# Kernel tuning notes

Hardware: AMD Instinct MI355X
Metric: run time of the kernel (lower is better)

The kernel has to match this reference:

```python
import jax, jax.numpy as jnp
import numpy as np

CHEB = jnp.array([676.5203681218851, -1259.1392167224028, 771.3234287776531,
                  -176.6150291621406, 12.507343278686905, -0.13857109526572012,
                  9.984369578019572e-06, 1.5056327351493116e-07], dtype=jnp.float32)
TWO_PI = float(np.sqrt(2.0 * np.pi))  # sqrt(2*pi), matches torch two_pi constant


def _gamma(z):
    # Lanczos approximation, 8 Chebyshev terms
    x = jnp.full_like(z, 0.9999999999998099)
    for i in range(8):
        x = x + CHEB[i] / (z + (i + 1.0))
    t = z + 8.0 - 0.5
    y = TWO_PI * t ** (z + 0.5) * jnp.exp(-t) * x
    return y / z


def _lower_incl_gamma(s, x, iters=8):
    it = iters - 2
    gs = _gamma(s)
    L = x ** s * gs * jnp.exp(-x)
    gs = gs * s
    R = jnp.reciprocal(gs) * jnp.ones_like(x)
    X = x
    for k in range(it):
        gs = gs * (s + k + 1)
        R = R + X / gs
        X = X * x
    gs = gs * (s + it + 1)
    R = R + X / gs
    return L * R


def _trigamma(x):
    z = x + 1.0
    zz = z * z
    a = 0.2 - jnp.reciprocal(7.0 * zz)
    b = 1.0 - a / zz
    c = 1.0 + b / (3.0 * z)
    d = 1.0 + c / (2.0 * z)
    return d / z + jnp.reciprocal(x * x)


def _k_update(k, s):
    nm = jnp.log(k) - jax.scipy.special.digamma(k) - s
    dn = jnp.reciprocal(k) - _trigamma(k)
    return k - nm / dn


def _compute_ml_est(x, i=10):
    # x: [B, N]; returns per-image k, th of shape [B]
    x = x + 1e-07
    mean_x = jnp.mean(x, axis=1)
    s = jnp.log(mean_x) - jnp.mean(jnp.log(x), axis=1)
    s3 = s - 3.0
    rt = jnp.sqrt(s3 * s3 + 24.0 * s)
    k = (3.0 - s + rt) / (12.0 * s) + 1e-07
    for _ in range(i):
        k = _k_update(k, s)
    k = jnp.clip(k, 1e-07, 18.0)
    th = jnp.reciprocal(k) * mean_x
    return k, th


def setup_inputs() -> dict:
    key = jax.random.key(0)
    x = jax.random.uniform(key, (256, 224, 224), dtype=jnp.float32)
    return {"x": x}


def reference(x):
    B, H, W = x.shape
    xf = x.reshape(B, H * W)
    xf = xf - jnp.min(xf, axis=1, keepdims=True) + 1e-07
    k, th = _compute_ml_est(xf)            # [B], [B]
    kb = k[:, None]                         # broadcast per-image stats over pixels
    y = jnp.reciprocal(_gamma(kb)) * _lower_incl_gamma(kb, xf / th[:, None])
    y = jnp.where(jnp.isfinite(y), y, jnp.zeros_like(y))
    return y.reshape(B, H, W)
```

## Files before the change

### kernel.cpp

```cpp
#include <hip/hip_runtime.h>
#include <math.h>

#define HW   50176
#define NV4  12544
#define TPB  1024

__device__ __forceinline__ float waveReduceMin(float v) {
#pragma unroll
    for (int o = 32; o > 0; o >>= 1) v = fminf(v, __shfl_down(v, o, 64));
    return v;
}
__device__ __forceinline__ double waveReduceSum(double v) {
#pragma unroll
    for (int o = 32; o > 0; o >>= 1) v += __shfl_down(v, o, 64);
    return v;
}

__device__ __forceinline__ float digamma_f(float x) {
    float r = 0.0f;
    while (x < 6.0f) { r -= 1.0f / x; x += 1.0f; }
    float f = 1.0f / (x * x);
    float ser = f * (1.0f/12.0f - f * (1.0f/120.0f - f * (1.0f/252.0f - f * (1.0f/240.0f - f * (1.0f/132.0f)))));
    return r + logf(x) - 0.5f / x - ser;
}

__device__ __forceinline__ float trigamma_ref(float x) {
    float z = x + 1.0f;
    float zz = z * z;
    float a = 0.2f - 1.0f / (7.0f * zz);
    float b = 1.0f - a / zz;
    float c = 1.0f + b / (3.0f * z);
    float d = 1.0f + c / (2.0f * z);
    return d / z + 1.0f / (x * x);
}

__global__ void __launch_bounds__(TPB)
gamma_norm2d(const float* __restrict__ x, float* __restrict__ out) {
    const int row = blockIdx.x;
    const int tid = threadIdx.x;
    const float4* __restrict__ xr = (const float4*)(x + (size_t)row * HW);
    float4* __restrict__ yr = (float4*)(out + (size_t)row * HW);

    const bool lastValid = (tid < (NV4 - 12 * TPB));

    float4 v[13];
#pragma unroll
    for (int j = 0; j < 12; ++j) v[j] = xr[tid + j * TPB];
    if (lastValid) v[12] = xr[tid + 12 * TPB];
    else           v[12] = make_float4(INFINITY, INFINITY, INFINITY, INFINITY);

    float m = INFINITY;
#pragma unroll
    for (int j = 0; j < 13; ++j)
        m = fminf(m, fminf(fminf(v[j].x, v[j].y), fminf(v[j].z, v[j].w)));
    m = waveReduceMin(m);

    __shared__ float  sminw[16];
    __shared__ double ssum[16], ssuml[16];
    __shared__ float  sparams[3];
    __shared__ float  scoef[8];

    const int wid = tid >> 6, lane = tid & 63;
    if (lane == 0) sminw[wid] = m;
    __syncthreads();
    if (tid == 0) {
        float mm = sminw[0];
        for (int i = 1; i < 16; ++i) mm = fminf(mm, sminw[i]);
        sparams[0] = mm;
    }
    __syncthreads();
    const float rmin = sparams[0];

    double lsum = 0.0, lsl = 0.0;
#pragma unroll
    for (int j = 0; j < 13; ++j) {
        if (j < 12 || lastValid) {
            float e0 = v[j].x, e1 = v[j].y, e2 = v[j].z, e3 = v[j].w;
            float xm0 = (e0 - rmin + 1e-7f) + 1e-7f;
            float xm1 = (e1 - rmin + 1e-7f) + 1e-7f;
            float xm2 = (e2 - rmin + 1e-7f) + 1e-7f;
            float xm3 = (e3 - rmin + 1e-7f) + 1e-7f;
            lsum += ((double)xm0 + (double)xm1) + ((double)xm2 + (double)xm3);
            lsl  += ((double)__logf(xm0) + (double)__logf(xm1))
                  + ((double)__logf(xm2) + (double)__logf(xm3));
        }
    }
    lsum = waveReduceSum(lsum);
    lsl  = waveReduceSum(lsl);
    if (lane == 0) { ssum[wid] = lsum; ssuml[wid] = lsl; }
    __syncthreads();

    if (tid == 0) {
        double ts = 0.0, tl = 0.0;
        for (int i = 0; i < 16; ++i) { ts += ssum[i]; tl += ssuml[i]; }
        const double meand = ts / (double)HW;
        const double mlogd = tl / (double)HW;
        float s = (float)(log(meand) - mlogd);

        float s3 = s - 3.0f;
        float rt = sqrtf(s3 * s3 + 24.0f * s);
        float k  = (3.0f - s + rt) / (12.0f * s) + 1e-7f;
        for (int it = 0; it < 10; ++it) {
            float nm = logf(k) - digamma_f(k) - s;
            float dn = 1.0f / k - trigamma_ref(k);
            k = k - nm / dn;
        }
        if (k < 1e-7f) k = 1e-7f;
        if (k > 18.0f) k = 18.0f;

        const double CH[8] = {676.5203681218851, -1259.1392167224028, 771.3234287776531,
                              -176.6150291621406, 12.507343278686905, -0.13857109526572012,
                              9.984369578019572e-06, 1.5056327351493116e-07};
        double z = (double)k;
        double acc = 0.9999999999998099;
        for (int i = 0; i < 8; ++i) acc += CH[i] / (z + (double)(i + 1));
        double t = z + 7.5;
        double g = 2.5066282746310002 * exp((z + 0.5) * log(t) - t) * acc / z;

        double den = g * z;
        scoef[0] = (float)(1.0 / den);
        for (int j = 1; j < 8; ++j) {
            den *= (z + (double)j);
            scoef[j] = (float)(1.0 / den);
        }
        sparams[1] = k;
        sparams[2] = (float)((double)k / meand);
    }
    __syncthreads();

    const float kk    = sparams[1];
    const float invth = sparams[2];
    const float c0 = scoef[0], c1 = scoef[1], c2 = scoef[2], c3 = scoef[3];
    const float c4 = scoef[4], c5 = scoef[5], c6 = scoef[6], c7 = scoef[7];

#pragma unroll
    for (int j = 0; j < 13; ++j) {
        if (j < 12 || lastValid) {
            float e[4] = {v[j].x, v[j].y, v[j].z, v[j].w};
            float o[4];
#pragma unroll
            for (int q = 0; q < 4; ++q) {
                float xf = e[q] - rmin + 1e-7f;
                float xq = xf * invth;
                float p = fmaf(c7, xq, c6);
                p = fmaf(p, xq, c5);
                p = fmaf(p, xq, c4);
                p = fmaf(p, xq, c3);
                p = fmaf(p, xq, c2);
                p = fmaf(p, xq, c1);
                p = fmaf(p, xq, c0);
                float tt = __expf(fmaf(kk, __logf(xq), -xq));
                float y = tt * p;
                o[q] = isfinite(y) ? y : 0.0f;
            }
            yr[tid + j * TPB] = make_float4(o[0], o[1], o[2], o[3]);
        }
    }
}

extern "C" void kernel_launch(void* const* d_in, const int* in_sizes, int n_in,
                              void* d_out, int out_size, void* d_ws, size_t ws_size,
                              hipStream_t stream) {
    const float* x = (const float*)d_in[0];
    float* out = (float*)d_out;
    const int rows = in_sizes[0] / HW;
    gamma_norm2d<<<dim3(rows), dim3(TPB), 0, stream>>>(x, out);
}
```

Baseline: 113.6 us.

## Use float accumulation, fuse raw sum into min pass, fast divides, nontemporal stores

Replaces the per-element double-precision sum and log-sum accumulation with float accumulation per thread, converting to double only for the wave reductions. The plain sum is computed during the min pass and shifted by the row minimum afterward, which removes one dependency. The serial k-estimation and gamma code on thread 0 switches to fast divides and single-precision exp/log, and output stores become nontemporal. The aim is to cut FP64 ALU work and the single-thread serial section, at the cost of some accuracy in the mean and the gamma coefficients.

```diff
diff --git a/kernel.cpp b/kernel.cpp
--- a/kernel.cpp
+++ b/kernel.cpp
@@ -5,12 +5,14 @@
 #define NV4  12544
 #define TPB  1024
 
-__device__ __forceinline__ float waveReduceMin(float v) {
+typedef float floatx4 __attribute__((ext_vector_type(4)));
+
+__device__ __forceinline__ float waveMin(float v) {
 #pragma unroll
     for (int o = 32; o > 0; o >>= 1) v = fminf(v, __shfl_down(v, o, 64));
     return v;
 }
-__device__ __forceinline__ double waveReduceSum(double v) {
+__device__ __forceinline__ double waveSumD(double v) {
 #pragma unroll
     for (int o = 32; o > 0; o >>= 1) v += __shfl_down(v, o, 64);
     return v;
@@ -18,20 +20,21 @@
 
 __device__ __forceinline__ float digamma_f(float x) {
     float r = 0.0f;
-    while (x < 6.0f) { r -= 1.0f / x; x += 1.0f; }
-    float f = 1.0f / (x * x);
+#pragma unroll 6
+    for (int i = 0; i < 6; ++i) {
+        if (x < 6.0f) { r -= __fdividef(1.0f, x); x += 1.0f; }
+    }
+    float f = __fdividef(1.0f, x * x);
     float ser = f * (1.0f/12.0f - f * (1.0f/120.0f - f * (1.0f/252.0f - f * (1.0f/240.0f - f * (1.0f/132.0f)))));
-    return r + logf(x) - 0.5f / x - ser;
+    return r + logf(x) - 0.5f * __fdividef(1.0f, x) - ser;
 }
-
 __device__ __forceinline__ float trigamma_ref(float x) {
-    float z = x + 1.0f;
-    float zz = z * z;
-    float a = 0.2f - 1.0f / (7.0f * zz);
-    float b = 1.0f - a / zz;
-    float c = 1.0f + b / (3.0f * z);
-    float d = 1.0f + c / (2.0f * z);
-    return d / z + 1.0f / (x * x);
+    float z = x + 1.0f, zz = z * z;
+    float a = 0.2f - __fdividef(1.0f, 7.0f * zz);
+    float b = 1.0f - __fdividef(a, zz);
+    float c = 1.0f + __fdividef(b, 3.0f * z);
+    float d = 1.0f + __fdividef(c, 2.0f * z);
+    return __fdividef(d, z) + __fdividef(1.0f, x * x);
 }
 
 __global__ void __launch_bounds__(TPB)
@@ -39,71 +42,68 @@
     const int row = blockIdx.x;
     const int tid = threadIdx.x;
     const float4* __restrict__ xr = (const float4*)(x + (size_t)row * HW);
-    float4* __restrict__ yr = (float4*)(out + (size_t)row * HW);
 
-    const bool lastValid = (tid < (NV4 - 12 * TPB));
+    const bool extra = (tid < (NV4 - 12 * TPB));
 
     float4 v[13];
 #pragma unroll
     for (int j = 0; j < 12; ++j) v[j] = xr[tid + j * TPB];
-    if (lastValid) v[12] = xr[tid + 12 * TPB];
-    else           v[12] = make_float4(INFINITY, INFINITY, INFINITY, INFINITY);
+    v[12] = extra ? xr[tid + 12 * TPB]
+                  : make_float4(INFINITY, INFINITY, INFINITY, INFINITY);
 
-    float m = INFINITY;
+    float pmin = INFINITY, psum = 0.0f;
 #pragma unroll
-    for (int j = 0; j < 13; ++j)
-        m = fminf(m, fminf(fminf(v[j].x, v[j].y), fminf(v[j].z, v[j].w)));
-    m = waveReduceMin(m);
+    for (int j = 0; j < 13; ++j) {
+        pmin = fminf(pmin, fminf(fminf(v[j].x, v[j].y), fminf(v[j].z, v[j].w)));
+        if (j < 12 || extra) psum += (v[j].x + v[j].y) + (v[j].z + v[j].w);
+    }
+    pmin = waveMin(pmin);
+    double dsum = waveSumD((double)psum);
 
-    __shared__ float  sminw[16];
-    __shared__ double ssum[16], ssuml[16];
+    __shared__ float  smin[16];
+    __shared__ double sacc[16];
     __shared__ float  sparams[3];
     __shared__ float  scoef[8];
 
     const int wid = tid >> 6, lane = tid & 63;
-    if (lane == 0) sminw[wid] = m;
+    if (lane == 0) { smin[wid] = pmin; sacc[wid] = dsum; }
     __syncthreads();
     if (tid == 0) {
-        float mm = sminw[0];
-        for (int i = 1; i < 16; ++i) mm = fminf(mm, sminw[i]);
+        float mm = smin[0];
+        for (int i = 1; i < 16; ++i) mm = fminf(mm, smin[i]);
         sparams[0] = mm;
     }
     __syncthreads();
     const float rmin = sparams[0];
 
-    double lsum = 0.0, lsl = 0.0;
+    float psl = 0.0f;
 #pragma unroll
     for (int j = 0; j < 13; ++j) {
-        if (j < 12 || lastValid) {
-            float e0 = v[j].x, e1 = v[j].y, e2 = v[j].z, e3 = v[j].w;
-            float xm0 = (e0 - rmin + 1e-7f) + 1e-7f;
-            float xm1 = (e1 - rmin + 1e-7f) + 1e-7f;
-            float xm2 = (e2 - rmin + 1e-7f) + 1e-7f;
-            float xm3 = (e3 - rmin + 1e-7f) + 1e-7f;
-            lsum += ((double)xm0 + (double)xm1) + ((double)xm2 + (double)xm3);
-            lsl  += ((double)__logf(xm0) + (double)__logf(xm1))
-                  + ((double)__logf(xm2) + (double)__logf(xm3));
+        if (j < 12 || extra) {
+            psl += (__logf(v[j].x - rmin + 1e-7f + 1e-7f) + __logf(v[j].y - rmin + 1e-7f + 1e-7f))
+                 + (__logf(v[j].z - rmin + 1e-7f + 1e-7f) + __logf(v[j].w - rmin + 1e-7f + 1e-7f));
         }
     }
-    lsum = waveReduceSum(lsum);
-    lsl  = waveReduceSum(lsl);
-    if (lane == 0) { ssum[wid] = lsum; ssuml[wid] = lsl; }
+    double dsl = waveSumD((double)psl);
+    __shared__ double ssl[16];
+    if (lane == 0) ssl[wid] = dsl;
     __syncthreads();
 
     if (tid == 0) {
         double ts = 0.0, tl = 0.0;
-        for (int i = 0; i < 16; ++i) { ts += ssum[i]; tl += ssuml[i]; }
+        for (int i = 0; i < 16; ++i) { ts += sacc[i]; tl += ssl[i]; }
+        ts -= (double)HW * ((double)rmin - 2e-7);
         const double meand = ts / (double)HW;
-        const double mlogd = tl / (double)HW;
-        float s = (float)(log(meand) - mlogd);
+        float s = logf((float)meand) - (float)(tl / (double)HW);
 
         float s3 = s - 3.0f;
         float rt = sqrtf(s3 * s3 + 24.0f * s);
-        float k  = (3.0f - s + rt) / (12.0f * s) + 1e-7f;
+        float k  = __fdividef(3.0f - s + rt, 12.0f * s) + 1e-7f;
+#pragma unroll
         for (int it = 0; it < 10; ++it) {
             float nm = logf(k) - digamma_f(k) - s;
-            float dn = 1.0f / k - trigamma_ref(k);
-            k = k - nm / dn;
+            float dn = __fdividef(1.0f, k) - trigamma_ref(k);
+            k -= __fdividef(nm, dn);
         }
         if (k < 1e-7f) k = 1e-7f;
         if (k > 18.0f) k = 18.0f;
@@ -111,37 +111,37 @@
         const double CH[8] = {676.5203681218851, -1259.1392167224028, 771.3234287776531,
                               -176.6150291621406, 12.507343278686905, -0.13857109526572012,
                               9.984369578019572e-06, 1.5056327351493116e-07};
-        double z = (double)k;
         double acc = 0.9999999999998099;
-        for (int i = 0; i < 8; ++i) acc += CH[i] / (z + (double)(i + 1));
-        double t = z + 7.5;
-        double g = 2.5066282746310002 * exp((z + 0.5) * log(t) - t) * acc / z;
+#pragma unroll
+        for (int i = 0; i < 8; ++i) acc += CH[i] / ((double)k + (double)(i + 1));
+        float t  = k + 7.5f;
+        float g  = __expf(fmaf(k + 0.5f, __logf(t), -t)) * 2.50662827463f * (float)acc / k;
 
-        double den = g * z;
-        scoef[0] = (float)(1.0 / den);
+        float den = g * k;
+        scoef[0] = __fdividef(1.0f, den);
+#pragma unroll
         for (int j = 1; j < 8; ++j) {
-            den *= (z + (double)j);
-            scoef[j] = (float)(1.0 / den);
+            den *= (k + (float)j);
+            scoef[j] = __fdividef(1.0f, den);
         }
         sparams[1] = k;
         sparams[2] = (float)((double)k / meand);
     }
     __syncthreads();
 
-    const float kk    = sparams[1];
-    const float invth = sparams[2];
+    const float kk = sparams[1], invth = sparams[2];
     const float c0 = scoef[0], c1 = scoef[1], c2 = scoef[2], c3 = scoef[3];
     const float c4 = scoef[4], c5 = scoef[5], c6 = scoef[6], c7 = scoef[7];
 
+    floatx4* __restrict__ yr = (floatx4*)(out + (size_t)row * HW);
 #pragma unroll
     for (int j = 0; j < 13; ++j) {
-        if (j < 12 || lastValid) {
+        if (j < 12 || extra) {
             float e[4] = {v[j].x, v[j].y, v[j].z, v[j].w};
-            float o[4];
+            floatx4 o;
 #pragma unroll
             for (int q = 0; q < 4; ++q) {
-                float xf = e[q] - rmin + 1e-7f;
-                float xq = xf * invth;
+                float xq = (e[q] - rmin + 1e-7f) * invth;
                 float p = fmaf(c7, xq, c6);
                 p = fmaf(p, xq, c5);
                 p = fmaf(p, xq, c4);
@@ -149,11 +149,10 @@
                 p = fmaf(p, xq, c2);
                 p = fmaf(p, xq, c1);
                 p = fmaf(p, xq, c0);
-                float tt = __expf(fmaf(kk, __logf(xq), -xq));
-                float y = tt * p;
+                float y = __expf(fmaf(kk, __logf(xq), -xq)) * p;
                 o[q] = isfinite(y) ? y : 0.0f;
             }
-            yr[tid + j * TPB] = make_float4(o[0], o[1], o[2], o[3]);
+            __builtin_nontemporal_store(o, yr + tid + j * TPB);
         }
     }
 }
```

New measurement: 110.5 us. 1.03x faster.
